# Kernel optimization log

Hardware: AMD Instinct MI355X
Metric: run time of the kernel (lower is better)

## Reference

```python
import jax, jax.numpy as jnp
import numpy as np

D_MODEL, D_STATE, D_CONV, D_INNER = 1024, 16, 4, 2048
BATCH, SEQLEN = 4, 2048


def setup_inputs() -> dict:
    key = jax.random.key(0)
    ks = jax.random.split(key, 8)
    x = jax.random.normal(ks[0], (BATCH, SEQLEN, D_MODEL), jnp.float32)
    W_in = jax.random.normal(ks[1], (D_MODEL, 2 * D_INNER), jnp.float32) / np.float32(np.sqrt(D_MODEL))
    conv_w = jax.random.normal(ks[2], (D_INNER, 1, D_CONV), jnp.float32) * np.float32(0.3)
    W_x = jax.random.normal(ks[3], (D_INNER, 2 * D_STATE), jnp.float32) / np.float32(np.sqrt(D_INNER))
    W_dt = jax.random.normal(ks[4], (D_STATE, D_INNER), jnp.float32) / np.float32(np.sqrt(D_STATE))
    b_dt = jax.random.normal(ks[5], (D_INNER,), jnp.float32) * np.float32(0.1)
    W_Bp = jax.random.normal(ks[6], (D_STATE, D_INNER), jnp.float32) / np.float32(np.sqrt(D_STATE))
    D_param = jnp.ones((D_INNER,), jnp.float32)
    W_out = jax.random.normal(ks[7], (D_INNER, D_MODEL), jnp.float32) / np.float32(np.sqrt(D_INNER))
    return {"x": x, "W_in": W_in, "conv_w": conv_w, "W_x": W_x,
            "W_dt": W_dt, "b_dt": b_dt, "W_Bp": W_Bp, "D_param": D_param,
            "W_out": W_out}


def _mamba_fwd(x, W_in, conv_w, W_x, W_dt, b_dt, W_Bp, D_param, W_out):
    B, L, _ = x.shape
    xz = x @ W_in                                   # [B,L,2*d_inner]
    xc, z = jnp.split(xz, 2, axis=-1)
    # causal depthwise conv1d (torch pads d_conv-1 both sides then slices [:L])
    xt = jnp.transpose(xc, (0, 2, 1))               # [B,d_inner,L]
    xt = jax.lax.conv_general_dilated(
        xt, conv_w,
        window_strides=(1,), padding=[(D_CONV - 1, 0)],
        dimension_numbers=("NCH", "OIH", "NCH"),
        feature_group_count=D_INNER)
    u = jax.nn.silu(jnp.transpose(xt, (0, 2, 1)))   # [B,L,d_inner]
    xp = u @ W_x                                    # [B,L,2*d_state]
    dt_raw, B_raw = jnp.split(xp, 2, axis=-1)
    dt = jax.nn.softplus(dt_raw @ W_dt + b_dt)      # [B,L,d_inner]
    Bp = B_raw @ W_Bp                               # [B,L,d_inner]
    dt = jnp.clip(dt, 1e-4, 1.0)
    # selective scan: h_t = h_{t-1}*(1-dt_t) + u_t*Bp_t (note: A is unused in source)
    ub = u * Bp
    def step(h, inp):
        d_t, ub_t = inp
        h = h * (1.0 - d_t) + ub_t
        return h, h
    _, ys = jax.lax.scan(step, jnp.zeros((B, D_INNER), x.dtype),
                         (jnp.transpose(dt, (1, 0, 2)), jnp.transpose(ub, (1, 0, 2))))
    y = jnp.transpose(ys, (1, 0, 2)) + D_param * u  # [B,L,d_inner]
    y = y * jax.nn.silu(z)
    return y @ W_out                                # [B,L,d_model]


def reference(x, W_in, conv_w, W_x, W_dt, b_dt, W_Bp, D_param, W_out):
    # dropout is identity in eval mode
    return _mamba_fwd(x, W_in, conv_w, W_x, W_dt, b_dt, W_Bp, D_param, W_out)
```

## Files before the change

kernel.cpp:

```cpp
#include <hip/hip_runtime.h>
#include <cstdint>
#include <cstddef>

#define DM   1024
#define DI   2048
#define SEQ  2048
#define NB   4
#define NTOK (NB*SEQ)
#define CCH  32
#define LC   (SEQ/CCH)
#define KS   8

typedef __attribute__((ext_vector_type(8))) short short8v;
typedef __attribute__((ext_vector_type(4))) float f32x4;
typedef unsigned short u16;
typedef unsigned int   u32;

__device__ __forceinline__ float silu_f(float x){ return x / (1.f + __expf(-x)); }

__device__ __forceinline__ float softplus_f(float x){
  return (x > 20.f) ? x : __logf(1.f + __expf(x));
}

__device__ __forceinline__ u16 f2bf(float f){
  union { float f; u32 u; } c; c.f = f;
  u32 u = c.u + 0x7FFFu + ((c.u >> 16) & 1u);
  return (u16)(u >> 16);
}
__device__ __forceinline__ float b2f(u16 b){
  union { u32 u; float f; } c; c.u = ((u32)b) << 16; return c.f;
}
__device__ __forceinline__ float lo2f(u32 v){ union { u32 u; float f; } c; c.u = v << 16; return c.f; }
__device__ __forceinline__ float hi2f(u32 v){ union { u32 u; float f; } c; c.u = v & 0xFFFF0000u; return c.f; }
__device__ __forceinline__ u32 pack2(float a, float b){ return (u32)f2bf(a) | ((u32)f2bf(b) << 16); }

__device__ __forceinline__ void gl16(const void* g, void* l){
  __builtin_amdgcn_global_load_lds((const __attribute__((address_space(1))) void*)g,
                                   (__attribute__((address_space(3))) void*)l, 16, 0, 0);
}

__global__ __launch_bounds__(256) void cvtk(const float4* __restrict__ in,
                                            u16* __restrict__ outp, int n4)
{
  int i = blockIdx.x * 256 + threadIdx.x;
  if (i < n4) {
    float4 v = in[i];
    *(uint2*)(outp + (size_t)i * 4) = make_uint2(pack2(v.x, v.y), pack2(v.z, v.w));
  }
}

__global__ __launch_bounds__(256) void transcvt(
    const float* __restrict__ W, u16* __restrict__ Wt, int R, int Cn)
{
  __shared__ float t[64][65];
  const int tid = threadIdx.x;
  const int bx = blockIdx.x, by = blockIdx.y;
  const int lr4 = tid >> 6;
  const int lc  = tid & 63;
  #pragma unroll
  for (int p = 0; p < 16; ++p) {
    int lr = p * 4 + lr4;
    t[lr][lc] = W[(size_t)(by * 64 + lr) * Cn + bx * 64 + lc];
  }
  __syncthreads();
  #pragma unroll
  for (int p = 0; p < 16; ++p) {
    int orr = p * 4 + lr4;
    Wt[(size_t)(bx * 64 + orr) * R + by * 64 + lc] = f2bf(t[lc][orr]);
  }
}

__global__ __launch_bounds__(256) void prep_smallw(
    const float* __restrict__ W_x, const float* __restrict__ W_dt,
    const float* __restrict__ W_Bp, u16* __restrict__ Wxt, u16* __restrict__ Wbig)
{
  int i = blockIdx.x * 256 + threadIdx.x;
  if (i < 32 * DI) {
    int j = i >> 11, c = i & (DI - 1);
    Wxt[i] = f2bf(W_x[c * 32 + j]);
  }
  int i2 = i - 32 * DI;
  if (i2 >= 0 && i2 < 2 * DI * 32) {
    int n = i2 >> 5, k = i2 & 31;
    float v;
    if (n < DI) v = (k < 16) ? W_dt[k * DI + n] : 0.f;
    else        v = (k >= 16) ? W_Bp[(k - 16) * DI + (n - DI)] : 0.f;
    Wbig[i2] = f2bf(v);
  }
}

template<int NT, int LOG_NBX, int OBF16>
__global__ __launch_bounds__(256, 2) void gemm2b(
    const u16* __restrict__ A, const u16* __restrict__ Bt,
    void* C0v, void* C1v, int K, int split, int ldc)
{
  __shared__ __align__(16) u16 Ab[2][128 * 64];
  __shared__ __align__(16) u16 Bb[2][128 * 64];
  const int tid = threadIdx.x, lane = tid & 63, w = tid >> 6;
  const int wm = w >> 1, wn = w & 1;
  const int id = blockIdx.x;
  const int xcd = id & 7, slot = id >> 3;
  const int bm = (xcd * 8 + (slot >> LOG_NBX)) * 128;
  const int bn = (slot & ((1 << LOG_NBX) - 1)) * 128;

  const int srow8 = tid >> 3;
  const int kc = ((tid & 7) ^ (srow8 & 7)) << 3;
  const u16* Ag = A  + (size_t)(bm + srow8) * K + kc;
  const u16* Bg = Bt + (size_t)(bn + srow8) * K + kc;

  const int lq = lane >> 4, l15 = lane & 15;
  const int co0 = ((lq    ) ^ (l15 & 7)) << 3;
  const int co1 = ((lq + 4) ^ (l15 & 7)) << 3;
  const int abase = (wm * 64 + l15) * 64;
  const int bbase = (wn * 64 + l15) * 64;

  f32x4 acc[4][4] = {};

  auto issue = [&](int t, int buf) {
    const size_t k0 = (size_t)t << 6;
    #pragma unroll
    for (int q = 0; q < 4; ++q)
      gl16(Ag + (size_t)(q * 32) * K + k0, &Ab[buf][q * 2048 + tid * 8]);
    #pragma unroll
    for (int q = 0; q < 4; ++q)
      gl16(Bg + (size_t)(q * 32) * K + k0, &Bb[buf][q * 2048 + tid * 8]);
  };
  auto compute = [&](int buf) {
    const u16* Ac = Ab[buf];
    const u16* Bc = Bb[buf];
    short8v af[4], bf[4];
    #pragma unroll
    for (int ks = 0; ks < 2; ++ks) {
      const int co = ks ? co1 : co0;
      #pragma unroll
      for (int i = 0; i < 4; ++i) af[i] = *(const short8v*)&Ac[abase + i * 1024 + co];
      #pragma unroll
      for (int j = 0; j < 4; ++j) bf[j] = *(const short8v*)&Bc[bbase + j * 1024 + co];
      __builtin_amdgcn_s_setprio(1);
      #pragma unroll
      for (int i = 0; i < 4; ++i)
        #pragma unroll
        for (int j = 0; j < 4; ++j)
          acc[i][j] = __builtin_amdgcn_mfma_f32_16x16x32_bf16(af[i], bf[j], acc[i][j], 0, 0, 0);
      __builtin_amdgcn_s_setprio(0);
    }
  };

  issue(0, 0); issue(1, 1);
  #pragma unroll 1
  for (int t = 0; t < NT; ++t) {
    if (t + 1 < NT) asm volatile("s_waitcnt vmcnt(8)" ::: "memory");
    else            asm volatile("s_waitcnt vmcnt(0)" ::: "memory");
    __builtin_amdgcn_s_barrier(); __builtin_amdgcn_sched_barrier(0);
    compute(t & 1);
    __builtin_amdgcn_s_barrier(); __builtin_amdgcn_sched_barrier(0);
    if (t + 2 < NT) issue(t + 2, t & 1);
  }

  const bool left = (bn < split);
  const int cb = bn - (left ? 0 : split) + wn * 64 + l15;
  const int rb = bm + wm * 64 + lq * 4;
  if (OBF16) {
    u16* Cp = (u16*)(left ? C0v : C1v);
    #pragma unroll
    for (int i = 0; i < 4; ++i)
      #pragma unroll
      for (int j = 0; j < 4; ++j)
        #pragma unroll
        for (int r = 0; r < 4; ++r)
          Cp[(size_t)(rb + i * 16 + r) * ldc + cb + j * 16] = f2bf(acc[i][j][r]);
  } else {
    float* Cp = (float*)(left ? C0v : C1v);
    #pragma unroll
    for (int i = 0; i < 4; ++i)
      #pragma unroll
      for (int j = 0; j < 4; ++j)
        #pragma unroll
        for (int r = 0; r < 4; ++r)
          Cp[(size_t)(rb + i * 16 + r) * ldc + cb + j * 16] = acc[i][j][r];
  }
}

__global__ __launch_bounds__(256) void xp_gemm(
    const u16* __restrict__ A, const u16* __restrict__ Bt, float* __restrict__ xpp)
{
  __shared__ __align__(16) u16 Asm[128 * 32];
  __shared__ __align__(16) u16 Bsm[32 * 32];
  const int tid = threadIdx.x, lane = tid & 63, w = tid >> 6;
  const int bm = blockIdx.x * 128;
  const int kbase = blockIdx.y * (DI / KS);
  f32x4 acc[2][2] = {};
  const int srow = w * 32 + (lane >> 2);
  const int soct = lane & 3;
  const u16* Ap = A + (size_t)(bm + srow) * DI + kbase + soct * 8;
  const u16* Bp = Bt + (size_t)(lane >> 2) * DI + kbase + soct * 8;
  u16* As0 = &Asm[w * 1024];

  for (int k0 = 0; k0 < DI / KS; k0 += 32) {
    gl16(Ap + k0,                      As0);
    gl16(Ap + k0 + (size_t)16 * DI,    As0 + 512);
    if (w == 0) {
      gl16(Bp + k0,                    Bsm);
      gl16(Bp + k0 + (size_t)16 * DI,  Bsm + 512);
    }
    __syncthreads();
    short8v af[2], bf[2];
    #pragma unroll
    for (int i = 0; i < 2; ++i)
      af[i] = *(const short8v*)&Asm[(w * 32 + i * 16 + (lane & 15)) * 32 + (lane >> 4) * 8];
    #pragma unroll
    for (int j = 0; j < 2; ++j)
      bf[j] = *(const short8v*)&Bsm[(j * 16 + (lane & 15)) * 32 + (lane >> 4) * 8];
    #pragma unroll
    for (int i = 0; i < 2; ++i)
      #pragma unroll
      for (int j = 0; j < 2; ++j)
        acc[i][j] = __builtin_amdgcn_mfma_f32_16x16x32_bf16(af[i], bf[j], acc[i][j], 0, 0, 0);
    __syncthreads();
  }
  float* op = xpp + (size_t)blockIdx.y * NTOK * 32;
  const int rb = bm + w * 32 + (lane >> 4) * 4;
  const int cb = lane & 15;
  #pragma unroll
  for (int i = 0; i < 2; ++i)
    #pragma unroll
    for (int j = 0; j < 2; ++j)
      #pragma unroll
      for (int r = 0; r < 4; ++r)
        op[(size_t)(rb + i * 16 + r) * 32 + cb + j * 16] = acc[i][j][r];
}

__global__ __launch_bounds__(256) void xp_reduce(
    const float* __restrict__ xpp, u16* __restrict__ xpb)
{
  int i = blockIdx.x * 256 + threadIdx.x;
  float s = 0.f;
  #pragma unroll
  for (int k = 0; k < KS; ++k) s += xpp[(size_t)k * NTOK * 32 + i];
  xpb[i] = f2bf(s);
}

__global__ __launch_bounds__(256) void dtub_gemm(
    const u16* __restrict__ A, const u16* __restrict__ Bt,
    const float* __restrict__ b_dt, const u16* __restrict__ u,
    u16* __restrict__ dt_out, u16* __restrict__ ub_out)
{
  __shared__ __align__(16) u16 Asm[128 * 32];
  __shared__ __align__(16) u16 Bsm[128 * 32];
  const int tid = threadIdx.x, lane = tid & 63, w = tid >> 6;
  const int wm = w >> 1, wn = w & 1;
  const int bm = blockIdx.y * 128, bn = blockIdx.x * 128;
  const int srow = w * 32 + (lane >> 2);
  const int soct = lane & 3;
  u16* As0 = &Asm[w * 1024];
  u16* Bs0 = &Bsm[w * 1024];
  gl16(A  + (size_t)(bm + srow) * 32 + soct * 8,       As0);
  gl16(A  + (size_t)(bm + srow) * 32 + soct * 8 + 512, As0 + 512);
  gl16(Bt + (size_t)(bn + srow) * 32 + soct * 8,       Bs0);
  gl16(Bt + (size_t)(bn + srow) * 32 + soct * 8 + 512, Bs0 + 512);
  __syncthreads();
  f32x4 acc[4][4] = {};
  short8v afr[4], bfr[4];
  #pragma unroll
  for (int i = 0; i < 4; ++i) {
    afr[i] = *(const short8v*)&Asm[(wm * 64 + i * 16 + (lane & 15)) * 32 + (lane >> 4) * 8];
    bfr[i] = *(const short8v*)&Bsm[(wn * 64 + i * 16 + (lane & 15)) * 32 + (lane >> 4) * 8];
  }
  #pragma unroll
  for (int i = 0; i < 4; ++i)
    #pragma unroll
    for (int j = 0; j < 4; ++j)
      acc[i][j] = __builtin_amdgcn_mfma_f32_16x16x32_bf16(afr[i], bfr[j], acc[i][j], 0, 0, 0);

  const int rb = bm + wm * 64 + (lane >> 4) * 4;
  const int cb = bn + wn * 64 + (lane & 15);
  if (bn < DI) {
    float bd[4];
    #pragma unroll
    for (int j = 0; j < 4; ++j) bd[j] = b_dt[cb + j * 16];
    #pragma unroll
    for (int i = 0; i < 4; ++i)
      #pragma unroll
      for (int j = 0; j < 4; ++j)
        #pragma unroll
        for (int r = 0; r < 4; ++r) {
          float sp = softplus_f(acc[i][j][r] + bd[j]);
          sp = fminf(fmaxf(sp, 1e-4f), 1.0f);
          dt_out[(size_t)(rb + i * 16 + r) * DI + cb + j * 16] = f2bf(sp);
        }
  } else {
    const int cn = cb - DI;
    #pragma unroll
    for (int i = 0; i < 4; ++i)
      #pragma unroll
      for (int j = 0; j < 4; ++j)
        #pragma unroll
        for (int r = 0; r < 4; ++r) {
          size_t off = (size_t)(rb + i * 16 + r) * DI + cn + j * 16;
          ub_out[off] = f2bf(b2f(u[off]) * acc[i][j][r]);
        }
  }
}

__global__ __launch_bounds__(256) void conv_silu_k(
    const u16* __restrict__ xc, const float* __restrict__ cw, u16* __restrict__ u)
{
  int idx = blockIdx.x * 256 + threadIdx.x;
  int c = (idx & (DI / 4 - 1)) << 2;
  int r = idx >> 9;
  int t = r & (SEQ - 1);
  float4 w0 = ((const float4*)cw)[c + 0];
  float4 w1 = ((const float4*)cw)[c + 1];
  float4 w2 = ((const float4*)cw)[c + 2];
  float4 w3 = ((const float4*)cw)[c + 3];
  const u16* base = xc + (size_t)r * DI + c;
  uint2 v = *(const uint2*)base;
  float a0 = w0.w * lo2f(v.x), a1 = w1.w * hi2f(v.x);
  float a2 = w2.w * lo2f(v.y), a3 = w3.w * hi2f(v.y);
  if (t >= 1) { v = *(const uint2*)(base - DI);
    a0 += w0.z * lo2f(v.x); a1 += w1.z * hi2f(v.x); a2 += w2.z * lo2f(v.y); a3 += w3.z * hi2f(v.y); }
  if (t >= 2) { v = *(const uint2*)(base - 2 * DI);
    a0 += w0.y * lo2f(v.x); a1 += w1.y * hi2f(v.x); a2 += w2.y * lo2f(v.y); a3 += w3.y * hi2f(v.y); }
  if (t >= 3) { v = *(const uint2*)(base - 3 * DI);
    a0 += w0.x * lo2f(v.x); a1 += w1.x * hi2f(v.x); a2 += w2.x * lo2f(v.y); a3 += w3.x * hi2f(v.y); }
  *(uint2*)(u + (size_t)r * DI + c) =
      make_uint2(pack2(silu_f(a0), silu_f(a1)), pack2(silu_f(a2), silu_f(a3)));
}

__global__ __launch_bounds__(256) void scan_p1(
    const u16* __restrict__ dt_, const u16* __restrict__ ub,
    float* __restrict__ P, float* __restrict__ S)
{
  int idx = blockIdx.x * 256 + threadIdx.x;
  int di = (idx & (DI / 4 - 1)) << 2;
  int bc = idx >> 9;
  int c  = bc & (CCH - 1);
  int b  = bc >> 5;
  size_t base = ((size_t)b * SEQ + (size_t)c * LC) * DI + di;
  float p0 = 1.f, s0 = 0.f, p1 = 1.f, s1 = 0.f;
  float p2 = 1.f, s2 = 0.f, p3 = 1.f, s3 = 0.f;
  #pragma unroll 4
  for (int t = 0; t < LC; ++t) {
    size_t off = base + (size_t)t * DI;
    uint2 dv = *(const uint2*)(dt_ + off);
    uint2 uv = *(const uint2*)(ub + off);
    float a0 = 1.f - lo2f(dv.x), a1 = 1.f - hi2f(dv.x);
    float a2 = 1.f - lo2f(dv.y), a3 = 1.f - hi2f(dv.y);
    s0 = s0 * a0 + lo2f(uv.x); p0 *= a0;
    s1 = s1 * a1 + hi2f(uv.x); p1 *= a1;
    s2 = s2 * a2 + lo2f(uv.y); p2 *= a2;
    s3 = s3 * a3 + hi2f(uv.y); p3 *= a3;
  }
  ((float4*)P)[idx] = make_float4(p0, p1, p2, p3);
  ((float4*)S)[idx] = make_float4(s0, s1, s2, s3);
}

__global__ __launch_bounds__(256) void scan_p2(
    const float* __restrict__ P, const float* __restrict__ S, float* __restrict__ Hin)
{
  int idx = blockIdx.x * 256 + threadIdx.x;
  int di = idx & (DI - 1);
  int b  = idx >> 11;
  float h = 0.f;
  #pragma unroll
  for (int c = 0; c < CCH; ++c) {
    size_t off = ((size_t)b * CCH + c) * DI + di;
    Hin[off] = h;
    h = h * P[off] + S[off];
  }
}

__global__ __launch_bounds__(256) void scan_p3(
    const u16* dt_, const u16* __restrict__ ub, const u16* __restrict__ u,
    const u16* __restrict__ z, const float* __restrict__ Dp_,
    const float* __restrict__ Hin, u16* y)
{
  int idx = blockIdx.x * 256 + threadIdx.x;
  int di = (idx & (DI / 4 - 1)) << 2;
  int bc = idx >> 9;
  int c  = bc & (CCH - 1);
  int b  = bc >> 5;
  float4 dp = ((const float4*)Dp_)[di >> 2];
  float4 h4 = ((const float4*)Hin)[idx];
  float h0 = h4.x, h1 = h4.y, h2 = h4.z, h3 = h4.w;
  size_t base = ((size_t)b * SEQ + (size_t)c * LC) * DI + di;
  #pragma unroll 4
  for (int t = 0; t < LC; ++t) {
    size_t off = base + (size_t)t * DI;
    uint2 dv = *(const uint2*)(dt_ + off);
    uint2 uv = *(const uint2*)(ub + off);
    uint2 uu = *(const uint2*)(u + off);
    uint2 zv = *(const uint2*)(z + off);
    h0 = h0 * (1.f - lo2f(dv.x)) + lo2f(uv.x);
    h1 = h1 * (1.f - hi2f(dv.x)) + hi2f(uv.x);
    h2 = h2 * (1.f - lo2f(dv.y)) + lo2f(uv.y);
    h3 = h3 * (1.f - hi2f(dv.y)) + hi2f(uv.y);
    float y0 = (h0 + dp.x * lo2f(uu.x)) * silu_f(lo2f(zv.x));
    float y1 = (h1 + dp.y * hi2f(uu.x)) * silu_f(hi2f(zv.x));
    float y2 = (h2 + dp.z * lo2f(uu.y)) * silu_f(lo2f(zv.y));
    float y3 = (h3 + dp.w * hi2f(uu.y)) * silu_f(hi2f(zv.y));
    *(uint2*)(y + off) = make_uint2(pack2(y0, y1), pack2(y2, y3));
  }
}

extern "C" void kernel_launch(void* const* d_in, const int* in_sizes, int n_in,
                              void* d_out, int out_size, void* d_ws, size_t ws_size,
                              hipStream_t stream)
{
  const float* x     = (const float*)d_in[0];
  const float* W_in  = (const float*)d_in[1];
  const float* cw    = (const float*)d_in[2];
  const float* W_x   = (const float*)d_in[3];
  const float* W_dt  = (const float*)d_in[4];
  const float* b_dt  = (const float*)d_in[5];
  const float* W_Bp  = (const float*)d_in[6];
  const float* Dp    = (const float*)d_in[7];
  const float* W_out = (const float*)d_in[8];
  float* out = (float*)d_out;

  const size_t SZ = (size_t)NTOK * DI;
  float* w    = (float*)d_ws;
  float* bufA = w;
  float* bufB = w + SZ;
  float* bufC = w + 2 * SZ;
  float* bufD = w + 3 * SZ;

  u16* xcb  = (u16*)bufA;
  u16* zb   = (u16*)bufB;
  u16* wtob = zb + (size_t)NTOK * DI;
  u16* wxt  = wtob + (size_t)DM * DI;
  u16* wbig = wxt + (size_t)32 * DI;
  u16* xbf  = (u16*)bufC;
  u16* wtib = xbf + (size_t)NTOK * DM;
  u16* ubf  = (u16*)bufC;
  u16* ubb  = (u16*)bufD;

  const size_t PS = (size_t)NB * CCH * DI;
  float* Pbuf   = out;
  float* Sbuf   = out + PS;
  float* Hin    = out + 2 * PS;
  float* xppart = out + 3 * PS;
  u16*   xpb    = (u16*)(out + 3 * PS + (size_t)KS * NTOK * 32);
  (void)ws_size; (void)in_sizes; (void)n_in; (void)out_size;

  cvtk<<<(NTOK * DM / 4) / 256, 256, 0, stream>>>((const float4*)x, xbf, NTOK * DM / 4);
  transcvt<<<dim3((2 * DI) / 64, DM / 64), 256, 0, stream>>>(W_in, wtib, DM, 2 * DI);
  transcvt<<<dim3(DM / 64, DI / 64), 256, 0, stream>>>(W_out, wtob, DI, DM);
  prep_smallw<<<(32 * DI + 2 * DI * 32) / 256, 256, 0, stream>>>(W_x, W_dt, W_Bp, wxt, wbig);

  gemm2b<DM / 64, 5, 1><<<2048, 256, 0, stream>>>(
      xbf, wtib, (void*)xcb, (void*)zb, DM, DI, DI);

  conv_silu_k<<<(NTOK * DI / 4) / 256, 256, 0, stream>>>(xcb, cw, ubf);

  xp_gemm<<<dim3(NTOK / 128, KS), 256, 0, stream>>>(ubf, wxt, xppart);
  xp_reduce<<<(NTOK * 32) / 256, 256, 0, stream>>>(xppart, xpb);
  dtub_gemm<<<dim3((2 * DI) / 128, NTOK / 128), 256, 0, stream>>>(
      xpb, wbig, b_dt, ubf, xcb, ubb);

  scan_p1<<<(NB * CCH * DI / 4) / 256, 256, 0, stream>>>(xcb, ubb, Pbuf, Sbuf);
  scan_p2<<<(NB * DI) / 256, 256, 0, stream>>>(Pbuf, Sbuf, Hin);
  scan_p3<<<(NB * CCH * DI / 4) / 256, 256, 0, stream>>>(xcb, ubb, ubf, zb, Dp, Hin, xcb);

  gemm2b<DI / 64, 3, 0><<<512, 256, 0, stream>>>(
      xcb, wtob, (void*)out, (void*)out, DI, DM, DM);
}
```

Before: 307.6 us.

## Shrink GEMM K-tile to 32, raise occupancy, drop XCD-aware block swizzle

The main bf16 GEMM kernel now stages K-tiles of 32 instead of 64, which halves shared memory per block, and launch bounds rise to 3 blocks per CU. The XCD-aware 1D block remapping is replaced by a plain 2D grid, and the LDS swizzle is reworked for the narrower rows. The aim is more latency hiding through occupancy. In exchange there are twice as many barrier-separated iterations with less MFMA work each, and the loss of the swizzle may hurt L2 locality across XCDs.

Measured after the change: 308.7 us. Within noise of the previous version (+0.3%).

```diff
diff --git a/kernel.cpp b/kernel.cpp
--- a/kernel.cpp
+++ b/kernel.cpp
@@ -89,67 +89,57 @@
   }
 }
 
-template<int NT, int LOG_NBX, int OBF16>
-__global__ __launch_bounds__(256, 2) void gemm2b(
+template<int NT, int OBF16>
+__global__ __launch_bounds__(256, 3) void gemm2b(
     const u16* __restrict__ A, const u16* __restrict__ Bt,
     void* C0v, void* C1v, int K, int split, int ldc)
 {
-  __shared__ __align__(16) u16 Ab[2][128 * 64];
-  __shared__ __align__(16) u16 Bb[2][128 * 64];
+  __shared__ __align__(16) u16 Ab[2][128 * 32];
+  __shared__ __align__(16) u16 Bb[2][128 * 32];
   const int tid = threadIdx.x, lane = tid & 63, w = tid >> 6;
   const int wm = w >> 1, wn = w & 1;
-  const int id = blockIdx.x;
-  const int xcd = id & 7, slot = id >> 3;
-  const int bm = (xcd * 8 + (slot >> LOG_NBX)) * 128;
-  const int bn = (slot & ((1 << LOG_NBX) - 1)) * 128;
-
-  const int srow8 = tid >> 3;
-  const int kc = ((tid & 7) ^ (srow8 & 7)) << 3;
-  const u16* Ag = A  + (size_t)(bm + srow8) * K + kc;
-  const u16* Bg = Bt + (size_t)(bn + srow8) * K + kc;
+  const int bm = blockIdx.y * 128, bn = blockIdx.x * 128;
+
+  const int srow = tid >> 2;
+  const int kc = ((tid & 3) ^ ((srow >> 1) & 3)) << 3;
+  const u16* Ag = A  + (size_t)(bm + srow) * K + kc;
+  const u16* Bg = Bt + (size_t)(bn + srow) * K + kc;
 
   const int lq = lane >> 4, l15 = lane & 15;
-  const int co0 = ((lq    ) ^ (l15 & 7)) << 3;
-  const int co1 = ((lq + 4) ^ (l15 & 7)) << 3;
-  const int abase = (wm * 64 + l15) * 64;
-  const int bbase = (wn * 64 + l15) * 64;
+  const int co = ((lq ^ ((l15 >> 1) & 3)) << 3);
+  const int abase = (wm * 64 + l15) * 32;
+  const int bbase = (wn * 64 + l15) * 32;
 
   f32x4 acc[4][4] = {};
 
   auto issue = [&](int t, int buf) {
-    const size_t k0 = (size_t)t << 6;
-    #pragma unroll
-    for (int q = 0; q < 4; ++q)
-      gl16(Ag + (size_t)(q * 32) * K + k0, &Ab[buf][q * 2048 + tid * 8]);
-    #pragma unroll
-    for (int q = 0; q < 4; ++q)
-      gl16(Bg + (size_t)(q * 32) * K + k0, &Bb[buf][q * 2048 + tid * 8]);
+    const size_t k0 = (size_t)t << 5;
+    gl16(Ag + k0,                    &Ab[buf][tid * 8]);
+    gl16(Ag + (size_t)64 * K + k0,   &Ab[buf][2048 + tid * 8]);
+    gl16(Bg + k0,                    &Bb[buf][tid * 8]);
+    gl16(Bg + (size_t)64 * K + k0,   &Bb[buf][2048 + tid * 8]);
   };
   auto compute = [&](int buf) {
     const u16* Ac = Ab[buf];
     const u16* Bc = Bb[buf];
     short8v af[4], bf[4];
     #pragma unroll
-    for (int ks = 0; ks < 2; ++ks) {
-      const int co = ks ? co1 : co0;
-      #pragma unroll
-      for (int i = 0; i < 4; ++i) af[i] = *(const short8v*)&Ac[abase + i * 1024 + co];
-      #pragma unroll
-      for (int j = 0; j < 4; ++j) bf[j] = *(const short8v*)&Bc[bbase + j * 1024 + co];
-      __builtin_amdgcn_s_setprio(1);
-      #pragma unroll
-      for (int i = 0; i < 4; ++i)
-        #pragma unroll
-        for (int j = 0; j < 4; ++j)
-          acc[i][j] = __builtin_amdgcn_mfma_f32_16x16x32_bf16(af[i], bf[j], acc[i][j], 0, 0, 0);
-      __builtin_amdgcn_s_setprio(0);
-    }
+    for (int i = 0; i < 4; ++i) af[i] = *(const short8v*)&Ac[abase + i * 512 + co];
+    #pragma unroll
+    for (int j = 0; j < 4; ++j) bf[j] = *(const short8v*)&Bc[bbase + j * 512 + co];
+    __builtin_amdgcn_s_setprio(1);
+    #pragma unroll
+    for (int i = 0; i < 4; ++i)
+      #pragma unroll
+      for (int j = 0; j < 4; ++j)
+        acc[i][j] = __builtin_amdgcn_mfma_f32_16x16x32_bf16(af[i], bf[j], acc[i][j], 0, 0, 0);
+    __builtin_amdgcn_s_setprio(0);
   };
 
   issue(0, 0); issue(1, 1);
   #pragma unroll 1
   for (int t = 0; t < NT; ++t) {
-    if (t + 1 < NT) asm volatile("s_waitcnt vmcnt(8)" ::: "memory");
+    if (t + 1 < NT) asm volatile("s_waitcnt vmcnt(4)" ::: "memory");
     else            asm volatile("s_waitcnt vmcnt(0)" ::: "memory");
     __builtin_amdgcn_s_barrier(); __builtin_amdgcn_sched_barrier(0);
     compute(t & 1);
@@ -448,7 +438,7 @@
   transcvt<<<dim3(DM / 64, DI / 64), 256, 0, stream>>>(W_out, wtob, DI, DM);
   prep_smallw<<<(32 * DI + 2 * DI * 32) / 256, 256, 0, stream>>>(W_x, W_dt, W_Bp, wxt, wbig);
 
-  gemm2b<DM / 64, 5, 1><<<2048, 256, 0, stream>>>(
+  gemm2b<DM / 32, 1><<<dim3((2 * DI) / 128, NTOK / 128), 256, 0, stream>>>(
       xbf, wtib, (void*)xcb, (void*)zb, DM, DI, DI);
 
   conv_silu_k<<<(NTOK * DI / 4) / 256, 256, 0, stream>>>(xcb, cw, ubf);
@@ -462,6 +452,6 @@
   scan_p2<<<(NB * DI) / 256, 256, 0, stream>>>(Pbuf, Sbuf, Hin);
   scan_p3<<<(NB * CCH * DI / 4) / 256, 256, 0, stream>>>(xcb, ubb, ubf, zb, Dp, Hin, xcb);
 
-  gemm2b<DI / 64, 3, 0><<<512, 256, 0, stream>>>(
+  gemm2b<DI / 32, 0><<<dim3(DM / 128, NTOK / 128), 256, 0, stream>>>(
       xcb, wtob, (void*)out, (void*)out, DI, DM, DM);
 }
```

## Fuse split-K reduction into dtub_gemm and drop XCD-aware GEMM block swizzle

Applied to the files above, without the earlier changes.

Removes the separate xp_reduce kernel and has dtub_gemm sum the KS fp32 partials directly while staging its A tile into shared memory, converting to bf16 there. It also replaces the XCD-aware block index remapping in gemm2b with a plain 2D grid. Fusing saves one launch and a round trip through global memory for the reduced xp. The cost is that each of the 32 column blocks of dtub_gemm now re-reads all KS partials for its rows. Dropping the swizzle may lose L2 locality across XCDs.

Measured after the change: 308.2 us. About the same (+0.2%).

```diff
diff --git a/kernel.cpp b/kernel.cpp
--- a/kernel.cpp
+++ b/kernel.cpp
@@ -89,7 +89,7 @@
   }
 }
 
-template<int NT, int LOG_NBX, int OBF16>
+template<int NT, int OBF16>
 __global__ __launch_bounds__(256, 2) void gemm2b(
     const u16* __restrict__ A, const u16* __restrict__ Bt,
     void* C0v, void* C1v, int K, int split, int ldc)
@@ -98,10 +98,7 @@
   __shared__ __align__(16) u16 Bb[2][128 * 64];
   const int tid = threadIdx.x, lane = tid & 63, w = tid >> 6;
   const int wm = w >> 1, wn = w & 1;
-  const int id = blockIdx.x;
-  const int xcd = id & 7, slot = id >> 3;
-  const int bm = (xcd * 8 + (slot >> LOG_NBX)) * 128;
-  const int bn = (slot & ((1 << LOG_NBX) - 1)) * 128;
+  const int bm = blockIdx.y * 128, bn = blockIdx.x * 128;
 
   const int srow8 = tid >> 3;
   const int kc = ((tid & 7) ^ (srow8 & 7)) << 3;
@@ -230,18 +227,8 @@
         op[(size_t)(rb + i * 16 + r) * 32 + cb + j * 16] = acc[i][j][r];
 }
 
-__global__ __launch_bounds__(256) void xp_reduce(
-    const float* __restrict__ xpp, u16* __restrict__ xpb)
-{
-  int i = blockIdx.x * 256 + threadIdx.x;
-  float s = 0.f;
-  #pragma unroll
-  for (int k = 0; k < KS; ++k) s += xpp[(size_t)k * NTOK * 32 + i];
-  xpb[i] = f2bf(s);
-}
-
 __global__ __launch_bounds__(256) void dtub_gemm(
-    const u16* __restrict__ A, const u16* __restrict__ Bt,
+    const float* __restrict__ xpp, const u16* __restrict__ Bt,
     const float* __restrict__ b_dt, const u16* __restrict__ u,
     u16* __restrict__ dt_out, u16* __restrict__ ub_out)
 {
@@ -252,12 +239,32 @@
   const int bm = blockIdx.y * 128, bn = blockIdx.x * 128;
   const int srow = w * 32 + (lane >> 2);
   const int soct = lane & 3;
-  u16* As0 = &Asm[w * 1024];
   u16* Bs0 = &Bsm[w * 1024];
-  gl16(A  + (size_t)(bm + srow) * 32 + soct * 8,       As0);
-  gl16(A  + (size_t)(bm + srow) * 32 + soct * 8 + 512, As0 + 512);
   gl16(Bt + (size_t)(bn + srow) * 32 + soct * 8,       Bs0);
   gl16(Bt + (size_t)(bn + srow) * 32 + soct * 8 + 512, Bs0 + 512);
+
+  {
+    const int arow = tid >> 1;
+    const int ach  = (tid & 1) * 16;
+    float s[16];
+    #pragma unroll
+    for (int e = 0; e < 16; ++e) s[e] = 0.f;
+    const float* xp0 = xpp + (size_t)(bm + arow) * 32 + ach;
+    #pragma unroll
+    for (int k = 0; k < KS; ++k) {
+      const float4* p = (const float4*)(xp0 + (size_t)k * NTOK * 32);
+      #pragma unroll
+      for (int q = 0; q < 4; ++q) {
+        float4 v = p[q];
+        s[q*4+0] += v.x; s[q*4+1] += v.y; s[q*4+2] += v.z; s[q*4+3] += v.w;
+      }
+    }
+    u32 pk[8];
+    #pragma unroll
+    for (int q = 0; q < 8; ++q) pk[q] = pack2(s[2*q], s[2*q+1]);
+    *(uint4*)&Asm[arow * 32 + ach]     = make_uint4(pk[0], pk[1], pk[2], pk[3]);
+    *(uint4*)&Asm[arow * 32 + ach + 8] = make_uint4(pk[4], pk[5], pk[6], pk[7]);
+  }
   __syncthreads();
   f32x4 acc[4][4] = {};
   short8v afr[4], bfr[4];
@@ -440,7 +447,6 @@
   float* Sbuf   = out + PS;
   float* Hin    = out + 2 * PS;
   float* xppart = out + 3 * PS;
-  u16*   xpb    = (u16*)(out + 3 * PS + (size_t)KS * NTOK * 32);
   (void)ws_size; (void)in_sizes; (void)n_in; (void)out_size;
 
   cvtk<<<(NTOK * DM / 4) / 256, 256, 0, stream>>>((const float4*)x, xbf, NTOK * DM / 4);
@@ -448,20 +454,19 @@
   transcvt<<<dim3(DM / 64, DI / 64), 256, 0, stream>>>(W_out, wtob, DI, DM);
   prep_smallw<<<(32 * DI + 2 * DI * 32) / 256, 256, 0, stream>>>(W_x, W_dt, W_Bp, wxt, wbig);
 
-  gemm2b<DM / 64, 5, 1><<<2048, 256, 0, stream>>>(
+  gemm2b<DM / 64, 1><<<dim3((2 * DI) / 128, NTOK / 128), 256, 0, stream>>>(
       xbf, wtib, (void*)xcb, (void*)zb, DM, DI, DI);
 
   conv_silu_k<<<(NTOK * DI / 4) / 256, 256, 0, stream>>>(xcb, cw, ubf);
 
   xp_gemm<<<dim3(NTOK / 128, KS), 256, 0, stream>>>(ubf, wxt, xppart);
-  xp_reduce<<<(NTOK * 32) / 256, 256, 0, stream>>>(xppart, xpb);
   dtub_gemm<<<dim3((2 * DI) / 128, NTOK / 128), 256, 0, stream>>>(
-      xpb, wbig, b_dt, ubf, xcb, ubb);
+      xppart, wbig, b_dt, ubf, xcb, ubb);
 
   scan_p1<<<(NB * CCH * DI / 4) / 256, 256, 0, stream>>>(xcb, ubb, Pbuf, Sbuf);
   scan_p2<<<(NB * DI) / 256, 256, 0, stream>>>(Pbuf, Sbuf, Hin);
   scan_p3<<<(NB * CCH * DI / 4) / 256, 256, 0, stream>>>(xcb, ubb, ubf, zb, Dp, Hin, xcb);
 
-  gemm2b<DI / 64, 3, 0><<<512, 256, 0, stream>>>(
+  gemm2b<DI / 64, 0><<<dim3(DM / 128, NTOK / 128), 256, 0, stream>>>(
       xcb, wtob, (void*)out, (void*)out, DI, DM, DM);
 }
```

## Fuse prep kernels into one launch and use plain 2D GEMM grid

Applied to the files above, without the earlier changes.

Merges the input conversion, both weight transpose-converts and the small-weight prep into a single kernel that dispatches on block index, cutting several launches. The GEMM drops its XCD-aware block index remapping and uses a direct 2D grid for tile coordinates. This simplifies scheduling but risks worse L2 reuse across the chiplet dies, since tiles sharing rows may no longer land on the same XCD.

Result: faster. 293.0 us (-4.8%).

```diff
diff --git a/kernel.cpp b/kernel.cpp
--- a/kernel.cpp
+++ b/kernel.cpp
@@ -39,22 +39,15 @@
                                    (__attribute__((address_space(3))) void*)l, 16, 0, 0);
 }
 
-__global__ __launch_bounds__(256) void cvtk(const float4* __restrict__ in,
-                                            u16* __restrict__ outp, int n4)
-{
-  int i = blockIdx.x * 256 + threadIdx.x;
-  if (i < n4) {
-    float4 v = in[i];
-    *(uint2*)(outp + (size_t)i * 4) = make_uint2(pack2(v.x, v.y), pack2(v.z, v.w));
-  }
-}
-
-__global__ __launch_bounds__(256) void transcvt(
-    const float* __restrict__ W, u16* __restrict__ Wt, int R, int Cn)
-{
-  __shared__ float t[64][65];
-  const int tid = threadIdx.x;
-  const int bx = blockIdx.x, by = blockIdx.y;
+#define PREP_CVT   8192
+#define PREP_T1    (PREP_CVT + 1024)
+#define PREP_T2    (PREP_T1 + 512)
+#define PREP_TOTAL (PREP_T2 + 768)
+
+__device__ void transcvt_dev(const float* __restrict__ W, u16* __restrict__ Wt,
+                             int R, int Cn, int bx, int by, int tid,
+                             float (*t)[65])
+{
   const int lr4 = tid >> 6;
   const int lc  = tid & 63;
   #pragma unroll
@@ -70,26 +63,43 @@
   }
 }
 
-__global__ __launch_bounds__(256) void prep_smallw(
+__global__ __launch_bounds__(256) void prep_all(
+    const float* __restrict__ x, u16* __restrict__ xbf,
+    const float* __restrict__ W_in, u16* __restrict__ wtib,
+    const float* __restrict__ W_out, u16* __restrict__ wtob,
     const float* __restrict__ W_x, const float* __restrict__ W_dt,
     const float* __restrict__ W_Bp, u16* __restrict__ Wxt, u16* __restrict__ Wbig)
 {
-  int i = blockIdx.x * 256 + threadIdx.x;
-  if (i < 32 * DI) {
-    int j = i >> 11, c = i & (DI - 1);
-    Wxt[i] = f2bf(W_x[c * 32 + j]);
-  }
-  int i2 = i - 32 * DI;
-  if (i2 >= 0 && i2 < 2 * DI * 32) {
-    int n = i2 >> 5, k = i2 & 31;
-    float v;
-    if (n < DI) v = (k < 16) ? W_dt[k * DI + n] : 0.f;
-    else        v = (k >= 16) ? W_Bp[(k - 16) * DI + (n - DI)] : 0.f;
-    Wbig[i2] = f2bf(v);
-  }
-}
-
-template<int NT, int LOG_NBX, int OBF16>
+  __shared__ float t[64][65];
+  const int bid = blockIdx.x, tid = threadIdx.x;
+  if (bid < PREP_CVT) {
+    int i = bid * 256 + tid;
+    float4 v = ((const float4*)x)[i];
+    *(uint2*)(xbf + (size_t)i * 4) = make_uint2(pack2(v.x, v.y), pack2(v.z, v.w));
+  } else if (bid < PREP_T1) {
+    int r = bid - PREP_CVT;
+    transcvt_dev(W_in, wtib, DM, 2 * DI, r & 63, r >> 6, tid, t);
+  } else if (bid < PREP_T2) {
+    int r = bid - PREP_T1;
+    transcvt_dev(W_out, wtob, DI, DM, r & 15, r >> 4, tid, t);
+  } else {
+    int i = (bid - PREP_T2) * 256 + tid;
+    if (i < 32 * DI) {
+      int j = i >> 11, c = i & (DI - 1);
+      Wxt[i] = f2bf(W_x[c * 32 + j]);
+    }
+    int i2 = i - 32 * DI;
+    if (i2 >= 0 && i2 < 2 * DI * 32) {
+      int n = i2 >> 5, k = i2 & 31;
+      float v;
+      if (n < DI) v = (k < 16) ? W_dt[k * DI + n] : 0.f;
+      else        v = (k >= 16) ? W_Bp[(k - 16) * DI + (n - DI)] : 0.f;
+      Wbig[i2] = f2bf(v);
+    }
+  }
+}
+
+template<int NT, int OBF16>
 __global__ __launch_bounds__(256, 2) void gemm2b(
     const u16* __restrict__ A, const u16* __restrict__ Bt,
     void* C0v, void* C1v, int K, int split, int ldc)
@@ -98,10 +108,7 @@
   __shared__ __align__(16) u16 Bb[2][128 * 64];
   const int tid = threadIdx.x, lane = tid & 63, w = tid >> 6;
   const int wm = w >> 1, wn = w & 1;
-  const int id = blockIdx.x;
-  const int xcd = id & 7, slot = id >> 3;
-  const int bm = (xcd * 8 + (slot >> LOG_NBX)) * 128;
-  const int bn = (slot & ((1 << LOG_NBX) - 1)) * 128;
+  const int bm = blockIdx.y * 128, bn = blockIdx.x * 128;
 
   const int srow8 = tid >> 3;
   const int kc = ((tid & 7) ^ (srow8 & 7)) << 3;
@@ -443,12 +450,10 @@
   u16*   xpb    = (u16*)(out + 3 * PS + (size_t)KS * NTOK * 32);
   (void)ws_size; (void)in_sizes; (void)n_in; (void)out_size;
 
-  cvtk<<<(NTOK * DM / 4) / 256, 256, 0, stream>>>((const float4*)x, xbf, NTOK * DM / 4);
-  transcvt<<<dim3((2 * DI) / 64, DM / 64), 256, 0, stream>>>(W_in, wtib, DM, 2 * DI);
-  transcvt<<<dim3(DM / 64, DI / 64), 256, 0, stream>>>(W_out, wtob, DI, DM);
-  prep_smallw<<<(32 * DI + 2 * DI * 32) / 256, 256, 0, stream>>>(W_x, W_dt, W_Bp, wxt, wbig);
-
-  gemm2b<DM / 64, 5, 1><<<2048, 256, 0, stream>>>(
+  prep_all<<<PREP_TOTAL, 256, 0, stream>>>(
+      x, xbf, W_in, wtib, W_out, wtob, W_x, W_dt, W_Bp, wxt, wbig);
+
+  gemm2b<DM / 64, 1><<<dim3((2 * DI) / 128, NTOK / 128), 256, 0, stream>>>(
       xbf, wtib, (void*)xcb, (void*)zb, DM, DI, DI);
 
   conv_silu_k<<<(NTOK * DI / 4) / 256, 256, 0, stream>>>(xcb, cw, ubf);
@@ -462,6 +467,6 @@
   scan_p2<<<(NB * DI) / 256, 256, 0, stream>>>(Pbuf, Sbuf, Hin);
   scan_p3<<<(NB * CCH * DI / 4) / 256, 256, 0, stream>>>(xcb, ubb, ubf, zb, Dp, Hin, xcb);
 
-  gemm2b<DI / 64, 3, 0><<<512, 256, 0, stream>>>(
+  gemm2b<DI / 64, 0><<<dim3(DM / 128, NTOK / 128), 256, 0, stream>>>(
       xcb, wtob, (void*)out, (void*)out, DI, DM, DM);
 }
```
